# Kernel tuning notes

Measured on AMD Instinct MI355X. Metric: run time of the kernel, lower is better.

The kernel has to match this reference:

```python
import jax, jax.numpy as jnp
import numpy as np

H = 16          # num_heads
W = 256         # sliding window size
LN_EPS = 1e-6
ROPE_BASE = 10000.0


def layer_norm(x, g, b):
    m = jnp.mean(x, axis=-1, keepdims=True)
    v = jnp.mean((x - m) ** 2, axis=-1, keepdims=True)
    return (x - m) * jax.lax.rsqrt(v + LN_EPS) * g + b


def rope(x):
    # x: [B, S, H, hd]; rotate-half RoPE
    S, hd = x.shape[1], x.shape[-1]
    inv_freq = 1.0 / (ROPE_BASE ** (jnp.arange(0, hd, 2, dtype=jnp.float32) / hd))
    ang = jnp.arange(S, dtype=jnp.float32)[:, None] * inv_freq[None, :]  # [S, hd/2]
    cos = jnp.concatenate([jnp.cos(ang), jnp.cos(ang)], axis=-1)[None, :, None, :]
    sin = jnp.concatenate([jnp.sin(ang), jnp.sin(ang)], axis=-1)[None, :, None, :]
    x1, x2 = jnp.split(x, 2, axis=-1)
    rot = jnp.concatenate([-x2, x1], axis=-1)
    return x * cos + rot * sin


def setup_inputs() -> dict:
    key = jax.random.key(0)
    ks = jax.random.split(key, 12)
    B, S, D, I = 2, 2048, 1024, 4096
    s = 0.02
    return {
        "hidden_states": jax.random.normal(ks[0], (B, S, D), jnp.float32),
        "wq": jax.random.normal(ks[1], (D, D), jnp.float32) * s,
        "wk": jax.random.normal(ks[2], (D, D), jnp.float32) * s,
        "wv": jax.random.normal(ks[3], (D, D), jnp.float32) * s,
        "wo": jax.random.normal(ks[4], (D, D), jnp.float32) * s,
        "w1": jax.random.normal(ks[5], (D, I), jnp.float32) * s,
        "w2": jax.random.normal(ks[6], (I, D), jnp.float32) * s,
        "w3": jax.random.normal(ks[7], (D, I), jnp.float32) * s,
        "ln1_g": jnp.ones((D,), jnp.float32),
        "ln1_b": jnp.zeros((D,), jnp.float32),
        "ln2_g": jnp.ones((D,), jnp.float32),
        "ln2_b": jnp.zeros((D,), jnp.float32),
    }


def reference(hidden_states, wq, wk, wv, wo, w1, w2, w3, ln1_g, ln1_b, ln2_g, ln2_b):
    B, S, D = hidden_states.shape
    hd = D // H

    # --- attention sub-block ---
    residual = hidden_states
    x = layer_norm(hidden_states, ln1_g, ln1_b)
    q = (x @ wq).reshape(B, S, H, hd)
    k = (x @ wk).reshape(B, S, H, hd)
    v = (x @ wv).reshape(B, S, H, hd)
    q, k = rope(q), rope(k)

    scores = jnp.einsum("bqhd,bkhd->bhqk", q, k) / jnp.sqrt(jnp.float32(hd))
    idx = jnp.arange(S)
    rel = idx[:, None] - idx[None, :]          # i - j
    mask = (rel >= 0) & (rel < W)              # causal sliding window
    scores = jnp.where(mask[None, None], scores, jnp.float32(-1e9))
    attn = jax.nn.softmax(scores, axis=-1)
    ctx = jnp.einsum("bhqk,bkhd->bqhd", attn, v).reshape(B, S, D)
    hidden_states = residual + ctx @ wo

    # --- SwiGLU MLP sub-block ---
    residual = hidden_states
    x = layer_norm(hidden_states, ln2_g, ln2_b)
    mlp = (jax.nn.silu(x @ w1) * (x @ w3)) @ w2
    return residual + mlp
```

## Files before the change

### kernel.cpp

```cpp
#include <hip/hip_runtime.h>
#include <hip/hip_bf16.h>

typedef __bf16 bf16_t;
typedef __bf16 bf16x4 __attribute__((ext_vector_type(4)));
typedef __bf16 bf16x8 __attribute__((ext_vector_type(8)));
typedef float f32x4 __attribute__((ext_vector_type(4)));
typedef float f32x16 __attribute__((ext_vector_type(16)));

#define LN_EPS 1e-6f

__device__ __forceinline__ void gl2lds16(const void* g, void* l) {
    __builtin_amdgcn_global_load_lds(
        (const __attribute__((address_space(1))) void*)g,
        (__attribute__((address_space(3))) void*)l, 16, 0, 0);
}

__global__ void transpose_cvt_kernel(const float* __restrict__ in, bf16_t* __restrict__ out,
                                     int R, int C) {
    __shared__ float tile[32][33];
    int tx = threadIdx.x & 31;
    int ty = threadIdx.x >> 5;
    int r0 = blockIdx.y * 32;
    int c0 = blockIdx.x * 32;
#pragma unroll
    for (int i = 0; i < 4; i++) {
        int r = ty + i * 8;
        tile[r][tx] = in[(size_t)(r0 + r) * C + (c0 + tx)];
    }
    __syncthreads();
#pragma unroll
    for (int i = 0; i < 4; i++) {
        int r = ty + i * 8;
        out[(size_t)(c0 + r) * R + (r0 + tx)] = (bf16_t)tile[tx][r];
    }
}

__global__ void ln_kernel(const float* __restrict__ x, const float* __restrict__ g,
                          const float* __restrict__ bb, bf16_t* __restrict__ out, int D) {
    int row = blockIdx.x;
    int t = threadIdx.x;
    const float4* xr = reinterpret_cast<const float4*>(x + (size_t)row * D);
    float4 v = xr[t];
    float s = v.x + v.y + v.z + v.w;
    __shared__ float sbuf[4];
    __shared__ float sbuf2[4];
    int wave = t >> 6, lane = t & 63;
#pragma unroll
    for (int o = 32; o > 0; o >>= 1) s += __shfl_xor(s, o);
    if (lane == 0) sbuf[wave] = s;
    __syncthreads();
    float mean = (sbuf[0] + sbuf[1] + sbuf[2] + sbuf[3]) / (float)D;
    float d0 = v.x - mean, d1 = v.y - mean, d2 = v.z - mean, d3 = v.w - mean;
    float sq = d0 * d0 + d1 * d1 + d2 * d2 + d3 * d3;
#pragma unroll
    for (int o = 32; o > 0; o >>= 1) sq += __shfl_xor(sq, o);
    if (lane == 0) sbuf2[wave] = sq;
    __syncthreads();
    float var = (sbuf2[0] + sbuf2[1] + sbuf2[2] + sbuf2[3]) / (float)D;
    float inv = rsqrtf(var + LN_EPS);
    float4 gv = reinterpret_cast<const float4*>(g)[t];
    float4 bv = reinterpret_cast<const float4*>(bb)[t];
    bf16_t* o0 = out + (size_t)row * D + t * 4;
    o0[0] = (bf16_t)(d0 * inv * gv.x + bv.x);
    o0[1] = (bf16_t)(d1 * inv * gv.y + bv.y);
    o0[2] = (bf16_t)(d2 * inv * gv.z + bv.z);
    o0[3] = (bf16_t)(d3 * inv * gv.w + bv.w);
}

#define BM 128
#define BN 128
#define BKK 32

template <int EPI>
__launch_bounds__(256, 2) __global__
void gemm_kernel(const bf16_t* __restrict__ A, const bf16_t* __restrict__ Bt,
                 float* __restrict__ Cf, const float* __restrict__ aux,
                 const bf16_t* __restrict__ auxb, bf16_t* __restrict__ Cb,
                 int M, int N, int K) {
    __shared__ __align__(16) bf16_t As[BM * BKK];
    __shared__ __align__(16) bf16_t Bs[BN * BKK];
    int t = threadIdx.x;
    int lin = blockIdx.y * gridDim.x + blockIdx.x;
    int gmt = gridDim.y;
    int gw = 8 * gmt;
    int grp = lin / gw;
    int rem = lin - grp * gw;
    int bn = grp * 8 + (rem & 7);
    int bm = rem >> 3;
    int m0 = bm * BM;
    int n0 = bn * BN;
    int wave = t >> 6, lane = t & 63;
    int wm = (wave >> 1) * 64, wn = (wave & 1) * 64;
    int lr = lane & 15;
    int quad = lane >> 4;

    int srow = lane >> 2;
    int scol = (lane & 3) * 8;
    const bf16_t* ag = A + (size_t)(m0 + wave * 16 + srow) * K + scol;
    const bf16_t* bg = Bt + (size_t)(n0 + wave * 16 + srow) * K + scol;
    bf16_t* asl = As + wave * 16 * BKK;
    bf16_t* bsl = Bs + wave * 16 * BKK;
    const size_t rowskip = (size_t)64 * K;

    f32x4 acc[4][4];
#pragma unroll
    for (int mi = 0; mi < 4; mi++)
#pragma unroll
        for (int ni = 0; ni < 4; ni++) acc[mi][ni] = 0.f;

    for (int k0 = 0; k0 < K; k0 += BKK) {
        gl2lds16(ag + k0, asl);
        gl2lds16(ag + k0 + rowskip, asl + 64 * BKK);
        gl2lds16(bg + k0, bsl);
        gl2lds16(bg + k0 + rowskip, bsl + 64 * BKK);
        __syncthreads();
        bf16x8 af[4], bfv[4];
#pragma unroll
        for (int mi = 0; mi < 4; mi++)
            af[mi] = *reinterpret_cast<const bf16x8*>(&As[(wm + mi * 16 + lr) * BKK + quad * 8]);
#pragma unroll
        for (int ni = 0; ni < 4; ni++)
            bfv[ni] = *reinterpret_cast<const bf16x8*>(&Bs[(wn + ni * 16 + lr) * BKK + quad * 8]);
#pragma unroll
        for (int mi = 0; mi < 4; mi++)
#pragma unroll
            for (int ni = 0; ni < 4; ni++)
                acc[mi][ni] = __builtin_amdgcn_mfma_f32_16x16x32_bf16(af[mi], bfv[ni],
                                                                      acc[mi][ni], 0, 0, 0);
        __syncthreads();
    }
#pragma unroll
    for (int mi = 0; mi < 4; mi++) {
#pragma unroll
        for (int ni = 0; ni < 4; ni++) {
#pragma unroll
            for (int j = 0; j < 4; j++) {
                int gm = m0 + wm + mi * 16 + quad * 4 + j;
                int gn = n0 + wn + ni * 16 + lr;
                size_t idx = (size_t)gm * N + gn;
                float val = acc[mi][ni][j];
                if constexpr (EPI == 1) {
                    Cf[idx] = val + aux[idx];
                }
            }
        }
    }
}

#define G2_BM 256
#define G2_BN 128
#define G2_BK 32

template <int EPI>
__launch_bounds__(256, 2) __global__
void gemm2_kernel(const bf16_t* __restrict__ A, const bf16_t* __restrict__ Bt,
                  const bf16_t* __restrict__ auxb, bf16_t* __restrict__ Cb,
                  int M, int N, int K, int lda, int ldb) {
    __shared__ __align__(16) bf16_t As[G2_BM * G2_BK];
    __shared__ __align__(16) bf16_t Bs[G2_BN * G2_BK];
    int t = threadIdx.x;
    int wave = t >> 6, lane = t & 63;
    int m0 = blockIdx.x * G2_BM;
    int n0 = blockIdx.y * G2_BN;
    int koff = blockIdx.z * K;

    int sr = lane >> 2;
    int sq = (lane & 3) ^ (sr & 3);
    const bf16_t* ag = A + (size_t)(m0 + 64 * wave + sr) * lda + koff + sq * 8;
    const bf16_t* bg = Bt + (size_t)(n0 + 32 * wave + sr) * ldb + koff + sq * 8;
    bf16_t* asl = As + (64 * wave) * G2_BK;
    bf16_t* bsl = Bs + (32 * wave) * G2_BK;

    f32x16 acc[2][4];
#pragma unroll
    for (int mi = 0; mi < 2; mi++)
#pragma unroll
        for (int ni = 0; ni < 4; ni++) acc[mi][ni] = 0.f;

    int l31 = lane & 31;
    int lh = lane >> 5;
    int lx = lane & 3;

    for (int k0 = 0; k0 < K; k0 += G2_BK) {
#pragma unroll
        for (int i = 0; i < 4; i++)
            gl2lds16(ag + k0 + (size_t)(16 * i) * lda, asl + (16 * i) * G2_BK);
#pragma unroll
        for (int i = 0; i < 2; i++)
            gl2lds16(bg + k0 + (size_t)(16 * i) * ldb, bsl + (16 * i) * G2_BK);
        __syncthreads();
#pragma unroll
        for (int s = 0; s < 2; s++) {
            int q = 2 * s + lh;
            bf16x8 af[2], bfv[4];
#pragma unroll
            for (int mi = 0; mi < 2; mi++) {
                int row = 64 * wave + mi * 32 + l31;
                af[mi] = *reinterpret_cast<const bf16x8*>(&As[row * G2_BK + (q ^ lx) * 8]);
            }
#pragma unroll
            for (int ni = 0; ni < 4; ni++) {
                int row = ni * 32 + l31;
                bfv[ni] = *reinterpret_cast<const bf16x8*>(&Bs[row * G2_BK + (q ^ lx) * 8]);
            }
#pragma unroll
            for (int mi = 0; mi < 2; mi++)
#pragma unroll
                for (int ni = 0; ni < 4; ni++)
                    acc[mi][ni] = __builtin_amdgcn_mfma_f32_32x32x16_bf16(af[mi], bfv[ni],
                                                                          acc[mi][ni], 0, 0, 0);
        }
        __syncthreads();
    }

    if constexpr (EPI == 3) {
        const float kfreq = -0.41524101186f;
        bool do_rope = (n0 < 2048);
#pragma unroll
        for (int mi = 0; mi < 2; mi++) {
#pragma unroll
            for (int reg = 0; reg < 16; reg++) {
                int rrow = (reg & 3) + 8 * (reg >> 2) + 4 * lh;
                int gm = m0 + 64 * wave + mi * 32 + rrow;
                if (do_rope) {
                    float sf = (float)(gm & 2047);
                    float freq = exp2f((float)l31 * kfreq);
                    float ang = sf * freq;
                    float sn, cs;
                    __sincosf(ang, &sn, &cs);
#pragma unroll
                    for (int p = 0; p < 2; p++) {
                        float x1 = acc[mi][2 * p][reg];
                        float x2 = acc[mi][2 * p + 1][reg];
                        size_t idx = (size_t)gm * N + n0 + p * 64 + l31;
                        Cb[idx] = (bf16_t)(x1 * cs - x2 * sn);
                        Cb[idx + 32] = (bf16_t)(x2 * cs + x1 * sn);
                    }
                } else {
#pragma unroll
                    for (int ni = 0; ni < 4; ni++) {
                        size_t idx = (size_t)gm * N + n0 + ni * 32 + l31;
                        Cb[idx] = (bf16_t)acc[mi][ni][reg];
                    }
                }
            }
        }
    } else {
        size_t outoff = (EPI == 5) ? (size_t)blockIdx.z * M * N : 0;
#pragma unroll
        for (int mi = 0; mi < 2; mi++) {
#pragma unroll
            for (int reg = 0; reg < 16; reg++) {
                int rrow = (reg & 3) + 8 * (reg >> 2) + 4 * lh;
                int gm = m0 + 64 * wave + mi * 32 + rrow;
#pragma unroll
                for (int ni = 0; ni < 4; ni++) {
                    int gn = n0 + ni * 32 + l31;
                    size_t idx = (size_t)gm * N + gn;
                    float val = acc[mi][ni][reg];
                    if constexpr (EPI == 2) {
                        float a = (float)auxb[idx];
                        float sl = a / (1.0f + __expf(-a));
                        Cb[idx] = (bf16_t)(sl * val);
                    } else if constexpr (EPI == 4) {
                        Cb[idx] = (bf16_t)val;
                    } else if constexpr (EPI == 5) {
                        Cb[outoff + idx] = (bf16_t)val;
                    }
                }
            }
        }
    }
}

__global__ void reduce4_kernel(const bf16_t* __restrict__ p, const float* __restrict__ hid,
                               float* __restrict__ out, int n4) {
    int i = blockIdx.x * 256 + threadIdx.x;
    if (i >= n4) return;
    size_t i4 = (size_t)i * 4;
    float4 h = *reinterpret_cast<const float4*>(hid + i4);
    const size_t stride = (size_t)4096 * 1024;
#pragma unroll
    for (int c = 0; c < 4; c++) {
        bf16x4 a = *reinterpret_cast<const bf16x4*>(p + c * stride + i4);
        h.x += (float)a[0];
        h.y += (float)a[1];
        h.z += (float)a[2];
        h.w += (float)a[3];
    }
    *reinterpret_cast<float4*>(out + i4) = h;
}

__global__ void transpose_v_kernel(const bf16_t* __restrict__ v, bf16_t* __restrict__ vt,
                                   int S, int stride) {
    __shared__ bf16_t tile[64][66];
    int t = threadIdx.x;
    int s0 = blockIdx.x * 64;
    int h = blockIdx.y, b = blockIdx.z;
#pragma unroll
    for (int i = 0; i < 2; i++) {
        int c = t + i * 256;
        int ss = c >> 3, d8 = (c & 7) * 8;
        bf16x8 val = *reinterpret_cast<const bf16x8*>(
            &v[(size_t)(b * S + s0 + ss) * stride + h * 64 + d8]);
#pragma unroll
        for (int jj = 0; jj < 8; jj++) tile[ss][d8 + jj] = val[jj];
    }
    __syncthreads();
#pragma unroll
    for (int i = 0; i < 2; i++) {
        int c = t + i * 256;
        int d = c >> 3, s8 = (c & 7) * 8;
        bf16x8 o;
#pragma unroll
        for (int jj = 0; jj < 8; jj++) o[jj] = tile[s8 + jj][d];
        *reinterpret_cast<bf16x8*>(&vt[(((size_t)(b * 16 + h)) * 64 + d) * S + s0 + s8]) = o;
    }
}

#define PSTR 40
#define QKVS 3072
__global__ __launch_bounds__(256, 2) void attn_kernel(const bf16_t* __restrict__ qkv,
                                                      const bf16_t* __restrict__ vt,
                                                      bf16_t* __restrict__ ctx, int S) {
    __shared__ __align__(16) bf16_t Pbuf[4][16 * PSTR];
    int t = threadIdx.x;
    int wave = t >> 6, lane = t & 63;
    int col = lane & 15, quad = lane >> 4;
    int h = blockIdx.y, b = blockIdx.z;
    int q0 = blockIdx.x * 64 + wave * 16;

    const bf16_t* qrow = qkv + (size_t)(b * S + q0 + col) * QKVS + h * 64;
    bf16x8 aq0 = *reinterpret_cast<const bf16x8*>(qrow + quad * 8);
    bf16x8 aq1 = *reinterpret_cast<const bf16x8*>(qrow + 32 + quad * 8);

    int jbase = q0 - 256;
    f32x4 sc[18];
#pragma unroll
    for (int kt = 0; kt < 18; kt++) {
        int j = jbase + kt * 16 + col;
        int jc = j < 0 ? 0 : (j > S - 1 ? S - 1 : j);
        const bf16_t* krow = qkv + (size_t)(b * S + jc) * QKVS + 1024 + h * 64;
        bf16x8 bk0 = *reinterpret_cast<const bf16x8*>(krow + quad * 8);
        bf16x8 bk1 = *reinterpret_cast<const bf16x8*>(krow + 32 + quad * 8);
        f32x4 c0 = {0.f, 0.f, 0.f, 0.f};
        c0 = __builtin_amdgcn_mfma_f32_16x16x32_bf16(aq0, bk0, c0, 0, 0, 0);
        c0 = __builtin_amdgcn_mfma_f32_16x16x32_bf16(aq1, bk1, c0, 0, 0, 0);
        sc[kt] = c0;
    }
#pragma unroll
    for (int kt = 0; kt < 18; kt++) {
#pragma unroll
        for (int jj = 0; jj < 4; jj++) {
            int qq = quad * 4 + jj;
            int j = jbase + kt * 16 + col;
            int rel = (q0 + qq) - j;
            bool ok = (j >= 0) && (rel >= 0) && (rel < 256);
            sc[kt][jj] = ok ? sc[kt][jj] * 0.125f : -1e30f;
        }
    }
    float sminv[4];
#pragma unroll
    for (int jj = 0; jj < 4; jj++) {
        float m = -1e30f;
#pragma unroll
        for (int kt = 0; kt < 18; kt++) m = fmaxf(m, sc[kt][jj]);
#pragma unroll
        for (int o = 1; o < 16; o <<= 1) m = fmaxf(m, __shfl_xor(m, o));
        float s = 0.f;
#pragma unroll
        for (int kt = 0; kt < 18; kt++) {
            float p = __expf(sc[kt][jj] - m);
            sc[kt][jj] = p;
            s += p;
        }
#pragma unroll
        for (int o = 1; o < 16; o <<= 1) s += __shfl_xor(s, o);
        sminv[jj] = 1.0f / s;
    }
    f32x4 o[4];
#pragma unroll
    for (int n = 0; n < 4; n++) o[n] = 0.f;
    bf16_t* myP = Pbuf[wave];
    const bf16_t* vplane = vt + ((size_t)(b * 16 + h)) * 64 * S;
#pragma unroll
    for (int c = 0; c < 9; c++) {
#pragma unroll
        for (int half = 0; half < 2; half++) {
            int kt = 2 * c + half;
#pragma unroll
            for (int jj = 0; jj < 4; jj++) {
                int qq = quad * 4 + jj;
                myP[qq * PSTR + half * 16 + col] = (bf16_t)(sc[kt][jj] * sminv[jj]);
            }
        }
        bf16x8 ap = *reinterpret_cast<const bf16x8*>(myP + col * PSTR + quad * 8);
        int key0 = jbase + c * 32 + quad * 8;
        int kc = key0 < 0 ? 0 : (key0 > S - 8 ? S - 8 : key0);
#pragma unroll
        for (int n = 0; n < 4; n++) {
            bf16x8 bv = *reinterpret_cast<const bf16x8*>(vplane + ((size_t)(n * 16 + col)) * S + kc);
            o[n] = __builtin_amdgcn_mfma_f32_16x16x32_bf16(ap, bv, o[n], 0, 0, 0);
        }
    }
#pragma unroll
    for (int n = 0; n < 4; n++)
#pragma unroll
        for (int jj = 0; jj < 4; jj++) {
            int qq = quad * 4 + jj;
            ctx[((size_t)(b * S + q0 + qq) * 16 + h) * 64 + n * 16 + col] = (bf16_t)o[n][jj];
        }
}

extern "C" void kernel_launch(void* const* d_in, const int* in_sizes, int n_in,
                              void* d_out, int out_size, void* d_ws, size_t ws_size,
                              hipStream_t stream) {
    const float* hs   = (const float*)d_in[0];
    const float* wq   = (const float*)d_in[1];
    const float* wk   = (const float*)d_in[2];
    const float* wv   = (const float*)d_in[3];
    const float* wo   = (const float*)d_in[4];
    const float* w1   = (const float*)d_in[5];
    const float* w2   = (const float*)d_in[6];
    const float* w3   = (const float*)d_in[7];
    const float* ln1g = (const float*)d_in[8];
    const float* ln1b = (const float*)d_in[9];
    const float* ln2g = (const float*)d_in[10];
    const float* ln2b = (const float*)d_in[11];
    float* out = (float*)d_out;

    const int B = 2, S = 2048, D = 1024, I = 4096;
    const int BS = B * S;

    char* ws = (char*)d_ws;
    const size_t MB = 1024 * 1024;
    bf16_t* wq_t = (bf16_t*)(ws + 0 * MB);
    bf16_t* wk_t = (bf16_t*)(ws + 2 * MB);
    bf16_t* wv_t = (bf16_t*)(ws + 4 * MB);
    bf16_t* wo_t = (bf16_t*)(ws + 6 * MB);
    bf16_t* w1_t = (bf16_t*)(ws + 8 * MB);
    bf16_t* w3_t = (bf16_t*)(ws + 16 * MB);
    bf16_t* w2_t = (bf16_t*)(ws + 24 * MB);
    bf16_t* x_b  = (bf16_t*)(ws + 32 * MB);
    float*  hid  = (float*)(ws + 40 * MB);
    bf16_t* x2_b = (bf16_t*)(ws + 56 * MB);
    bf16_t* qkvb = (bf16_t*)(ws + 64 * MB);
    bf16_t* vt   = (bf16_t*)(ws + 88 * MB);
    bf16_t* ctxb = (bf16_t*)(ws + 96 * MB);
    bf16_t* h1b  = (bf16_t*)(ws + 64 * MB);
    bf16_t* hbuf = (bf16_t*)(ws + 96 * MB);
    bf16_t* pker = (bf16_t*)(ws + 64 * MB);

    dim3 tb(256);
    transpose_cvt_kernel<<<dim3(D / 32, D / 32), tb, 0, stream>>>(wq, wq_t, D, D);
    transpose_cvt_kernel<<<dim3(D / 32, D / 32), tb, 0, stream>>>(wk, wk_t, D, D);
    transpose_cvt_kernel<<<dim3(D / 32, D / 32), tb, 0, stream>>>(wv, wv_t, D, D);
    transpose_cvt_kernel<<<dim3(D / 32, D / 32), tb, 0, stream>>>(wo, wo_t, D, D);
    transpose_cvt_kernel<<<dim3(I / 32, D / 32), tb, 0, stream>>>(w1, w1_t, D, I);
    transpose_cvt_kernel<<<dim3(I / 32, D / 32), tb, 0, stream>>>(w3, w3_t, D, I);
    transpose_cvt_kernel<<<dim3(D / 32, I / 32), tb, 0, stream>>>(w2, w2_t, I, D);

    ln_kernel<<<BS, tb, 0, stream>>>(hs, ln1g, ln1b, x_b, D);

    gemm2_kernel<3><<<dim3(BS / G2_BM, 3072 / G2_BN), tb, 0, stream>>>(
        x_b, wq_t, nullptr, qkvb, BS, 3072, D, D, D);

    transpose_v_kernel<<<dim3(S / 64, 16, B), tb, 0, stream>>>(qkvb + 2048, vt, S, QKVS);

    attn_kernel<<<dim3(S / 64, 16, B), tb, 0, stream>>>(qkvb, vt, ctxb, S);

    gemm_kernel<1><<<dim3(D / BN, BS / BM), tb, 0, stream>>>(ctxb, wo_t, hid, hs, nullptr,
                                                             nullptr, BS, D, D);

    ln_kernel<<<BS, tb, 0, stream>>>(hid, ln2g, ln2b, x2_b, D);

    gemm2_kernel<4><<<dim3(BS / G2_BM, I / G2_BN), tb, 0, stream>>>(
        x2_b, w1_t, nullptr, h1b, BS, I, D, D, D);
    gemm2_kernel<2><<<dim3(BS / G2_BM, I / G2_BN), tb, 0, stream>>>(
        x2_b, w3_t, h1b, hbuf, BS, I, D, D, D);

    gemm2_kernel<5><<<dim3(BS / G2_BM, D / G2_BN, 4), tb, 0, stream>>>(
        hbuf, w2_t, nullptr, pker, BS, D, 1024, I, I);
    reduce4_kernel<<<dim3(BS * D / 4 / 256), tb, 0, stream>>>(pker, hid, out, BS * D / 4);
}
```

Before: 420.3 us.

## Pre-pack weights in k-group layout, load B from global, fuse w1/w3 GEMM

Weights are converted into a k-grouped packed layout of 8 bf16 per column, so the gemm2 kernel reads B fragments straight from global memory instead of staging them through LDS. The w1 and w3 weights are interleaved in 32-column groups, which lets a single GEMM compute both projections and apply SiLU-gate in its epilogue, removing the intermediate h1 buffer and one launch. The LDS swizzle for A changes to match. B reads now rely on L2 and cache hits rather than LDS reuse across waves, which could raise global traffic.

```diff
diff --git a/kernel.cpp b/kernel.cpp
--- a/kernel.cpp
+++ b/kernel.cpp
@@ -33,6 +33,28 @@
         int r = ty + i * 8;
         out[(size_t)(c0 + r) * R + (r0 + tx)] = (bf16_t)tile[tx][r];
     }
+}
+
+__global__ void interleave_cvt_kernel(const float* __restrict__ in, bf16_t* __restrict__ out,
+                                      int K, int Nw, int N_out, int noff, int mode) {
+    __shared__ bf16_t tile[32][72];
+    int t = threadIdx.x;
+    int k0 = blockIdx.y * 32, n0 = blockIdx.x * 64;
+    int c = t & 63;
+#pragma unroll
+    for (int i = 0; i < 8; i++) {
+        int r = (t >> 6) + i * 4;
+        tile[r][c] = (bf16_t)in[(size_t)(k0 + r) * Nw + n0 + c];
+    }
+    __syncthreads();
+    int kg = t >> 6;
+    int n = t & 63;
+    bf16x8 v;
+#pragma unroll
+    for (int j = 0; j < 8; j++) v[j] = tile[kg * 8 + j][n];
+    int gn = n0 + n;
+    int out_n = (mode == 1) ? ((gn >> 5) * 64 + (gn & 31) + noff) : (gn + noff);
+    *reinterpret_cast<bf16x8*>(out + ((size_t)(k0 >> 3) + kg) * N_out * 8 + (size_t)out_n * 8) = v;
 }
 
 __global__ void ln_kernel(const float* __restrict__ x, const float* __restrict__ g,
@@ -71,11 +93,9 @@
 #define BN 128
 #define BKK 32
 
-template <int EPI>
 __launch_bounds__(256, 2) __global__
 void gemm_kernel(const bf16_t* __restrict__ A, const bf16_t* __restrict__ Bt,
                  float* __restrict__ Cf, const float* __restrict__ aux,
-                 const bf16_t* __restrict__ auxb, bf16_t* __restrict__ Cb,
                  int M, int N, int K) {
     __shared__ __align__(16) bf16_t As[BM * BKK];
     __shared__ __align__(16) bf16_t Bs[BN * BKK];
@@ -130,21 +150,16 @@
         __syncthreads();
     }
 #pragma unroll
-    for (int mi = 0; mi < 4; mi++) {
-#pragma unroll
-        for (int ni = 0; ni < 4; ni++) {
+    for (int mi = 0; mi < 4; mi++)
+#pragma unroll
+        for (int ni = 0; ni < 4; ni++)
 #pragma unroll
             for (int j = 0; j < 4; j++) {
                 int gm = m0 + wm + mi * 16 + quad * 4 + j;
                 int gn = n0 + wn + ni * 16 + lr;
                 size_t idx = (size_t)gm * N + gn;
-                float val = acc[mi][ni][j];
-                if constexpr (EPI == 1) {
-                    Cf[idx] = val + aux[idx];
-                }
+                Cf[idx] = acc[mi][ni][j] + aux[idx];
             }
-        }
-    }
 }
 
 #define G2_BM 256
@@ -153,11 +168,9 @@
 
 template <int EPI>
 __launch_bounds__(256, 2) __global__
-void gemm2_kernel(const bf16_t* __restrict__ A, const bf16_t* __restrict__ Bt,
-                  const bf16_t* __restrict__ auxb, bf16_t* __restrict__ Cb,
-                  int M, int N, int K, int lda, int ldb) {
+void gemm2_kernel(const bf16_t* __restrict__ A, const bf16_t* __restrict__ Bw,
+                  bf16_t* __restrict__ Cb, int M, int N, int K, int lda) {
     __shared__ __align__(16) bf16_t As[G2_BM * G2_BK];
-    __shared__ __align__(16) bf16_t Bs[G2_BN * G2_BK];
     int t = threadIdx.x;
     int wave = t >> 6, lane = t & 63;
     int m0 = blockIdx.x * G2_BM;
@@ -165,11 +178,10 @@
     int koff = blockIdx.z * K;
 
     int sr = lane >> 2;
-    int sq = (lane & 3) ^ (sr & 3);
+    int sc = lane & 3;
+    int sq = sc ^ ((sr >> 1) & 3);
     const bf16_t* ag = A + (size_t)(m0 + 64 * wave + sr) * lda + koff + sq * 8;
-    const bf16_t* bg = Bt + (size_t)(n0 + 32 * wave + sr) * ldb + koff + sq * 8;
     bf16_t* asl = As + (64 * wave) * G2_BK;
-    bf16_t* bsl = Bs + (32 * wave) * G2_BK;
 
     f32x16 acc[2][4];
 #pragma unroll
@@ -179,37 +191,35 @@
 
     int l31 = lane & 31;
     int lh = lane >> 5;
-    int lx = lane & 3;
+    int rsw = (l31 >> 1) & 3;
 
     for (int k0 = 0; k0 < K; k0 += G2_BK) {
 #pragma unroll
         for (int i = 0; i < 4; i++)
             gl2lds16(ag + k0 + (size_t)(16 * i) * lda, asl + (16 * i) * G2_BK);
-#pragma unroll
-        for (int i = 0; i < 2; i++)
-            gl2lds16(bg + k0 + (size_t)(16 * i) * ldb, bsl + (16 * i) * G2_BK);
         __syncthreads();
+        bf16x8 bfv[2][4], af[2][2];
 #pragma unroll
         for (int s = 0; s < 2; s++) {
             int q = 2 * s + lh;
-            bf16x8 af[2], bfv[4];
-#pragma unroll
-            for (int mi = 0; mi < 2; mi++) {
-                int row = 64 * wave + mi * 32 + l31;
-                af[mi] = *reinterpret_cast<const bf16x8*>(&As[row * G2_BK + (q ^ lx) * 8]);
-            }
-#pragma unroll
-            for (int ni = 0; ni < 4; ni++) {
-                int row = ni * 32 + l31;
-                bfv[ni] = *reinterpret_cast<const bf16x8*>(&Bs[row * G2_BK + (q ^ lx) * 8]);
-            }
+            size_t qrow = ((size_t)((koff + k0) >> 3) + q) * N * 8;
+#pragma unroll
+            for (int ni = 0; ni < 4; ni++)
+                bfv[s][ni] = *reinterpret_cast<const bf16x8*>(
+                    Bw + qrow + (size_t)(n0 + ni * 32 + l31) * 8);
 #pragma unroll
             for (int mi = 0; mi < 2; mi++)
+                af[s][mi] = *reinterpret_cast<const bf16x8*>(
+                    &As[(64 * wave + mi * 32 + l31) * G2_BK + ((q ^ rsw) << 3)]);
+        }
+#pragma unroll
+        for (int s = 0; s < 2; s++)
+#pragma unroll
+            for (int mi = 0; mi < 2; mi++)
 #pragma unroll
                 for (int ni = 0; ni < 4; ni++)
-                    acc[mi][ni] = __builtin_amdgcn_mfma_f32_32x32x16_bf16(af[mi], bfv[ni],
-                                                                          acc[mi][ni], 0, 0, 0);
-        }
+                    acc[mi][ni] = __builtin_amdgcn_mfma_f32_32x32x16_bf16(
+                        af[s][mi], bfv[s][ni], acc[mi][ni], 0, 0, 0);
         __syncthreads();
     }
 
@@ -245,8 +255,8 @@
                 }
             }
         }
-    } else {
-        size_t outoff = (EPI == 5) ? (size_t)blockIdx.z * M * N : 0;
+    } else if constexpr (EPI == 6) {
+        int ldc = N >> 1;
 #pragma unroll
         for (int mi = 0; mi < 2; mi++) {
 #pragma unroll
@@ -254,20 +264,25 @@
                 int rrow = (reg & 3) + 8 * (reg >> 2) + 4 * lh;
                 int gm = m0 + 64 * wave + mi * 32 + rrow;
 #pragma unroll
-                for (int ni = 0; ni < 4; ni++) {
-                    int gn = n0 + ni * 32 + l31;
-                    size_t idx = (size_t)gm * N + gn;
-                    float val = acc[mi][ni][reg];
-                    if constexpr (EPI == 2) {
-                        float a = (float)auxb[idx];
-                        float sl = a / (1.0f + __expf(-a));
-                        Cb[idx] = (bf16_t)(sl * val);
-                    } else if constexpr (EPI == 4) {
-                        Cb[idx] = (bf16_t)val;
-                    } else if constexpr (EPI == 5) {
-                        Cb[outoff + idx] = (bf16_t)val;
-                    }
+                for (int p = 0; p < 2; p++) {
+                    float a1 = acc[mi][2 * p][reg];
+                    float a3 = acc[mi][2 * p + 1][reg];
+                    float sl = a1 / (1.0f + __expf(-a1));
+                    Cb[(size_t)gm * ldc + (n0 >> 1) + p * 32 + l31] = (bf16_t)(sl * a3);
                 }
+            }
+        }
+    } else {
+        size_t outoff = (size_t)blockIdx.z * M * N;
+#pragma unroll
+        for (int mi = 0; mi < 2; mi++) {
+#pragma unroll
+            for (int reg = 0; reg < 16; reg++) {
+                int rrow = (reg & 3) + 8 * (reg >> 2) + 4 * lh;
+                int gm = m0 + 64 * wave + mi * 32 + rrow;
+#pragma unroll
+                for (int ni = 0; ni < 4; ni++)
+                    Cb[outoff + (size_t)gm * N + n0 + ni * 32 + l31] = (bf16_t)acc[mi][ni][reg];
             }
         }
     }
@@ -434,52 +449,45 @@
 
     char* ws = (char*)d_ws;
     const size_t MB = 1024 * 1024;
-    bf16_t* wq_t = (bf16_t*)(ws + 0 * MB);
-    bf16_t* wk_t = (bf16_t*)(ws + 2 * MB);
-    bf16_t* wv_t = (bf16_t*)(ws + 4 * MB);
-    bf16_t* wo_t = (bf16_t*)(ws + 6 * MB);
-    bf16_t* w1_t = (bf16_t*)(ws + 8 * MB);
-    bf16_t* w3_t = (bf16_t*)(ws + 16 * MB);
-    bf16_t* w2_t = (bf16_t*)(ws + 24 * MB);
-    bf16_t* x_b  = (bf16_t*)(ws + 32 * MB);
-    float*  hid  = (float*)(ws + 40 * MB);
-    bf16_t* x2_b = (bf16_t*)(ws + 56 * MB);
-    bf16_t* qkvb = (bf16_t*)(ws + 64 * MB);
-    bf16_t* vt   = (bf16_t*)(ws + 88 * MB);
-    bf16_t* ctxb = (bf16_t*)(ws + 96 * MB);
-    bf16_t* h1b  = (bf16_t*)(ws + 64 * MB);
-    bf16_t* hbuf = (bf16_t*)(ws + 96 * MB);
-    bf16_t* pker = (bf16_t*)(ws + 64 * MB);
+    bf16_t* wo_t  = (bf16_t*)(ws + 0 * MB);
+    bf16_t* qkvw  = (bf16_t*)(ws + 2 * MB);
+    bf16_t* w13w  = (bf16_t*)(ws + 8 * MB);
+    bf16_t* w2w   = (bf16_t*)(ws + 24 * MB);
+    bf16_t* x_b   = (bf16_t*)(ws + 32 * MB);
+    float*  hid   = (float*)(ws + 40 * MB);
+    bf16_t* x2_b  = (bf16_t*)(ws + 56 * MB);
+    bf16_t* qkvb  = (bf16_t*)(ws + 64 * MB);
+    bf16_t* vt    = (bf16_t*)(ws + 88 * MB);
+    bf16_t* ctxb  = (bf16_t*)(ws + 96 * MB);
+    bf16_t* hbuf  = (bf16_t*)(ws + 64 * MB);
+    bf16_t* pker  = (bf16_t*)(ws + 96 * MB);
 
     dim3 tb(256);
-    transpose_cvt_kernel<<<dim3(D / 32, D / 32), tb, 0, stream>>>(wq, wq_t, D, D);
-    transpose_cvt_kernel<<<dim3(D / 32, D / 32), tb, 0, stream>>>(wk, wk_t, D, D);
-    transpose_cvt_kernel<<<dim3(D / 32, D / 32), tb, 0, stream>>>(wv, wv_t, D, D);
     transpose_cvt_kernel<<<dim3(D / 32, D / 32), tb, 0, stream>>>(wo, wo_t, D, D);
-    transpose_cvt_kernel<<<dim3(I / 32, D / 32), tb, 0, stream>>>(w1, w1_t, D, I);
-    transpose_cvt_kernel<<<dim3(I / 32, D / 32), tb, 0, stream>>>(w3, w3_t, D, I);
-    transpose_cvt_kernel<<<dim3(D / 32, I / 32), tb, 0, stream>>>(w2, w2_t, I, D);
+    interleave_cvt_kernel<<<dim3(D / 64, D / 32), tb, 0, stream>>>(wq, qkvw, D, D, 3072, 0, 0);
+    interleave_cvt_kernel<<<dim3(D / 64, D / 32), tb, 0, stream>>>(wk, qkvw, D, D, 3072, 1024, 0);
+    interleave_cvt_kernel<<<dim3(D / 64, D / 32), tb, 0, stream>>>(wv, qkvw, D, D, 3072, 2048, 0);
+    interleave_cvt_kernel<<<dim3(I / 64, D / 32), tb, 0, stream>>>(w1, w13w, D, I, 8192, 0, 1);
+    interleave_cvt_kernel<<<dim3(I / 64, D / 32), tb, 0, stream>>>(w3, w13w, D, I, 8192, 32, 1);
+    interleave_cvt_kernel<<<dim3(D / 64, I / 32), tb, 0, stream>>>(w2, w2w, I, D, 1024, 0, 0);
 
     ln_kernel<<<BS, tb, 0, stream>>>(hs, ln1g, ln1b, x_b, D);
 
     gemm2_kernel<3><<<dim3(BS / G2_BM, 3072 / G2_BN), tb, 0, stream>>>(
-        x_b, wq_t, nullptr, qkvb, BS, 3072, D, D, D);
+        x_b, qkvw, qkvb, BS, 3072, D, D);
 
     transpose_v_kernel<<<dim3(S / 64, 16, B), tb, 0, stream>>>(qkvb + 2048, vt, S, QKVS);
 
     attn_kernel<<<dim3(S / 64, 16, B), tb, 0, stream>>>(qkvb, vt, ctxb, S);
 
-    gemm_kernel<1><<<dim3(D / BN, BS / BM), tb, 0, stream>>>(ctxb, wo_t, hid, hs, nullptr,
-                                                             nullptr, BS, D, D);
+    gemm_kernel<<<dim3(D / BN, BS / BM), tb, 0, stream>>>(ctxb, wo_t, hid, hs, BS, D, D);
 
     ln_kernel<<<BS, tb, 0, stream>>>(hid, ln2g, ln2b, x2_b, D);
 
-    gemm2_kernel<4><<<dim3(BS / G2_BM, I / G2_BN), tb, 0, stream>>>(
-        x2_b, w1_t, nullptr, h1b, BS, I, D, D, D);
-    gemm2_kernel<2><<<dim3(BS / G2_BM, I / G2_BN), tb, 0, stream>>>(
-        x2_b, w3_t, h1b, hbuf, BS, I, D, D, D);
+    gemm2_kernel<6><<<dim3(BS / G2_BM, 8192 / G2_BN), tb, 0, stream>>>(
+        x2_b, w13w, hbuf, BS, 8192, D, D);
 
     gemm2_kernel<5><<<dim3(BS / G2_BM, D / G2_BN, 4), tb, 0, stream>>>(
-        hbuf, w2_t, nullptr, pker, BS, D, 1024, I, I);
+        hbuf, w2w, pker, BS, D, 1024, I);
     reduce4_kernel<<<dim3(BS * D / 4 / 256), tb, 0, stream>>>(pker, hid, out, BS * D / 4);
 }
```

Measured after the change: 436.9 us. 1.04x slower.
